# Performance work log

Measured on AMD Instinct MI355X. Metric: run time of the kernel, lower is better.

## Reference

```python
import jax, jax.numpy as jnp
import numpy as np

N_NODES = 100000
N_EDGES = 3200000
NCLASSES = 4
IN_DIM = 2          # per-node feature dim -> edge in_feats = 2*IN_DIM = 4
HID = 8             # output_dim


def setup_inputs() -> dict:
    key = jax.random.key(0)
    k_m, k_e, k_w1, k_b1, k_w2, k_b2 = jax.random.split(key, 6)
    m = jax.random.normal(k_m, (N_NODES, NCLASSES, IN_DIM), dtype=jnp.float32)
    edge_index = jax.random.randint(k_e, (2, N_EDGES), 0, N_NODES, dtype=jnp.int64)
    in_feats = 2 * IN_DIM
    # ClasswiseLinear: one independent Linear per class (grouped weights)
    s1 = 1.0 / np.sqrt(in_feats)
    s2 = 1.0 / np.sqrt(HID)
    W1 = jax.random.uniform(k_w1, (NCLASSES, in_feats, HID), jnp.float32, -s1, s1)
    b1 = jax.random.uniform(k_b1, (NCLASSES, HID), jnp.float32, -s1, s1)
    W2 = jax.random.uniform(k_w2, (NCLASSES, HID, 1), jnp.float32, -s2, s2)
    b2 = jax.random.uniform(k_b2, (NCLASSES, 1), jnp.float32, -s2, s2)
    return {"m": m, "edge_index": edge_index, "W1": W1, "b1": b1, "W2": W2, "b2": b2}


def reference(m, edge_index, W1, b1, W2, b2):
    row, col = edge_index[0], edge_index[1]
    # gather node features per edge; concat dest/src -> [E, C, 2*IN_DIM]
    B = jnp.concatenate([m[col], m[row]], axis=-1)
    B = jax.lax.stop_gradient(B)  # original code calls .detach()
    # classwise linear 1 + tanh: grouped GEMM over class axis c
    h = jnp.tanh(jnp.einsum("eci,cih->ech", B, W1) + b1)      # [E, C, HID]
    o = jnp.tanh(jnp.einsum("ech,cho->eco", h, W2) + b2)      # [E, C, 1]
    # softmax over the class dimension (dim=1)
    return jax.nn.softmax(o, axis=1)
```

## Files before the change

kernel.cpp:

```cpp
#include <hip/hip_runtime.h>

__device__ __forceinline__ float fast_tanh(float x) {
    float e = __builtin_amdgcn_exp2f(x * 2.8853901817779268f);
    float r = __builtin_amdgcn_rcpf(e + 1.0f);
    return fmaf(-2.0f, r, 1.0f);
}

__global__ __launch_bounds__(256) void edge_mlp(
    const float* __restrict__ m,
    const int*   __restrict__ eidx,
    const float* __restrict__ W1,
    const float* __restrict__ b1,
    const float* __restrict__ W2,
    const float* __restrict__ b2,
    float*       __restrict__ out,
    const int nE)
{
    const int tid0 = blockIdx.x * blockDim.x + threadIdx.x;
    const int c = tid0 & 3;

    float w1[32];
    #pragma unroll
    for (int k = 0; k < 8; ++k)
        *(float4*)(&w1[4*k]) = *(const float4*)(W1 + c*32 + 4*k);
    float bb1[8];
    *(float4*)(&bb1[0]) = *(const float4*)(b1 + c*8);
    *(float4*)(&bb1[4]) = *(const float4*)(b1 + c*8 + 4);
    float w2[8];
    *(float4*)(&w2[0]) = *(const float4*)(W2 + c*8);
    *(float4*)(&w2[4]) = *(const float4*)(W2 + c*8 + 4);
    const float b2s = b2[c];

    const int total  = nE * 4;
    const int stride = gridDim.x * blockDim.x;

    #pragma unroll 2
    for (int t = tid0; t < total; t += stride) {
        const int e   = t >> 2;
        const int row = eidx[e];
        const int col = eidx[nE + e];

        const float2 mc = *(const float2*)(m + (size_t)col * 8 + c * 2);
        const float2 mr = *(const float2*)(m + (size_t)row * 8 + c * 2);

        float o = b2s;
        #pragma unroll
        for (int j = 0; j < 8; ++j) {
            float h = bb1[j];
            h = fmaf(mc.x, w1[j],      h);
            h = fmaf(mc.y, w1[8 + j],  h);
            h = fmaf(mr.x, w1[16 + j], h);
            h = fmaf(mr.y, w1[24 + j], h);
            o = fmaf(fast_tanh(h), w2[j], o);
        }
        o = fast_tanh(o);

        const float eo = __builtin_amdgcn_exp2f(o * 1.4426950408889634f);
        float s = eo + __shfl_xor(eo, 1);
        s += __shfl_xor(s, 2);
        out[t] = eo * __builtin_amdgcn_rcpf(s);
    }
}

extern "C" void kernel_launch(void* const* d_in, const int* in_sizes, int n_in,
                              void* d_out, int out_size, void* d_ws, size_t ws_size,
                              hipStream_t stream) {
    const float* m  = (const float*)d_in[0];
    const int* eidx = (const int*)d_in[1];
    const float* W1 = (const float*)d_in[2];
    const float* b1 = (const float*)d_in[3];
    const float* W2 = (const float*)d_in[4];
    const float* b2 = (const float*)d_in[5];
    float* out = (float*)d_out;
    const int nE = in_sizes[1] / 2;

    const int threads = 256;
    const int blocks  = 2048;
    hipLaunchKernelGGL(edge_mlp, dim3(blocks), dim3(threads), 0, stream,
                       m, eidx, W1, b1, W2, b2, out, nE);
}
```

Before: 63.73 us.

## Process one edge per thread with all classes and vectorized node loads

Changes the mapping from one thread per (edge, class) to one thread per edge that computes all four classes. Each edge index is now loaded once instead of four times, node features are read as full float4 rows, and the output is written with a single nontemporal float4 store. The class softmax no longer needs cross-lane shuffles. Weights are now read from global memory as wave-uniform scalar loads rather than held per-lane in registers, and each thread does four times the arithmetic, which may raise register pressure and reduce available parallelism.

```diff
diff --git a/kernel.cpp b/kernel.cpp
--- a/kernel.cpp
+++ b/kernel.cpp
@@ -1,10 +1,9 @@
 #include <hip/hip_runtime.h>
 
-__device__ __forceinline__ float fast_tanh(float x) {
-    float e = __builtin_amdgcn_exp2f(x * 2.8853901817779268f);
-    float r = __builtin_amdgcn_rcpf(e + 1.0f);
-    return fmaf(-2.0f, r, 1.0f);
-}
+#define TWO_LOG2E 2.8853901817779268f
+#define LOG2E     1.4426950408889634f
+
+typedef float f32x4 __attribute__((ext_vector_type(4)));
 
 __global__ __launch_bounds__(256) void edge_mlp(
     const float* __restrict__ m,
@@ -16,49 +15,54 @@
     float*       __restrict__ out,
     const int nE)
 {
-    const int tid0 = blockIdx.x * blockDim.x + threadIdx.x;
-    const int c = tid0 & 3;
+    const int tid    = blockIdx.x * blockDim.x + threadIdx.x;
+    const int stride = gridDim.x * blockDim.x;
+    const int* eidx1 = eidx + nE;
 
-    float w1[32];
-    #pragma unroll
-    for (int k = 0; k < 8; ++k)
-        *(float4*)(&w1[4*k]) = *(const float4*)(W1 + c*32 + 4*k);
-    float bb1[8];
-    *(float4*)(&bb1[0]) = *(const float4*)(b1 + c*8);
-    *(float4*)(&bb1[4]) = *(const float4*)(b1 + c*8 + 4);
-    float w2[8];
-    *(float4*)(&w2[0]) = *(const float4*)(W2 + c*8);
-    *(float4*)(&w2[4]) = *(const float4*)(W2 + c*8 + 4);
-    const float b2s = b2[c];
+    for (int e0 = tid; e0 < nE; e0 += 2 * stride) {
+        #pragma unroll
+        for (int k = 0; k < 2; ++k) {
+            const int e = e0 + k * stride;
+            if (e >= nE) break;
+            const int r0 = __builtin_nontemporal_load(eidx  + e);
+            const int c0 = __builtin_nontemporal_load(eidx1 + e);
+            const f32x4 ca = *(const f32x4*)(m + (unsigned)c0 * 8u);
+            const f32x4 cb = *(const f32x4*)(m + (unsigned)c0 * 8u + 4);
+            const f32x4 ra = *(const f32x4*)(m + (unsigned)r0 * 8u);
+            const f32x4 rb = *(const f32x4*)(m + (unsigned)r0 * 8u + 4);
 
-    const int total  = nE * 4;
-    const int stride = gridDim.x * blockDim.x;
+            const float mcx[4] = {ca.x, ca.z, cb.x, cb.z};
+            const float mcy[4] = {ca.y, ca.w, cb.y, cb.w};
+            const float mrx[4] = {ra.x, ra.z, rb.x, rb.z};
+            const float mry[4] = {ra.y, ra.w, rb.y, rb.w};
 
-    #pragma unroll 2
-    for (int t = tid0; t < total; t += stride) {
-        const int e   = t >> 2;
-        const int row = eidx[e];
-        const int col = eidx[nE + e];
-
-        const float2 mc = *(const float2*)(m + (size_t)col * 8 + c * 2);
-        const float2 mr = *(const float2*)(m + (size_t)row * 8 + c * 2);
-
-        float o = b2s;
-        #pragma unroll
-        for (int j = 0; j < 8; ++j) {
-            float h = bb1[j];
-            h = fmaf(mc.x, w1[j],      h);
-            h = fmaf(mc.y, w1[8 + j],  h);
-            h = fmaf(mr.x, w1[16 + j], h);
-            h = fmaf(mr.y, w1[24 + j], h);
-            o = fmaf(fast_tanh(h), w2[j], o);
+            float eo[4];
+            float s = 0.0f;
+            #pragma unroll
+            for (int c = 0; c < 4; ++c) {
+                float o = b2[c];
+                #pragma unroll
+                for (int j = 0; j < 8; ++j) {
+                    float h = b1[c * 8 + j];
+                    h = fmaf(mcx[c], W1[c * 32 +      j], h);
+                    h = fmaf(mcy[c], W1[c * 32 +  8 + j], h);
+                    h = fmaf(mrx[c], W1[c * 32 + 16 + j], h);
+                    h = fmaf(mry[c], W1[c * 32 + 24 + j], h);
+                    const float ex = __builtin_amdgcn_exp2f(h * TWO_LOG2E);
+                    const float rr = __builtin_amdgcn_rcpf(ex + 1.0f);
+                    o = fmaf(fmaf(-2.0f, rr, 1.0f), W2[c * 8 + j], o);
+                }
+                const float e2 = __builtin_amdgcn_exp2f(o * TWO_LOG2E);
+                const float r2 = __builtin_amdgcn_rcpf(e2 + 1.0f);
+                eo[c] = __builtin_amdgcn_exp2f(fmaf(-TWO_LOG2E, r2, LOG2E));
+                s += eo[c];
+            }
+            const float rs = __builtin_amdgcn_rcpf(s);
+            f32x4 res;
+            res.x = eo[0] * rs; res.y = eo[1] * rs;
+            res.z = eo[2] * rs; res.w = eo[3] * rs;
+            __builtin_nontemporal_store(res, reinterpret_cast<f32x4*>(out) + e);
         }
-        o = fast_tanh(o);
-
-        const float eo = __builtin_amdgcn_exp2f(o * 1.4426950408889634f);
-        float s = eo + __shfl_xor(eo, 1);
-        s += __shfl_xor(s, 2);
-        out[t] = eo * __builtin_amdgcn_rcpf(s);
     }
 }
 
```

Result: slower. 70.18 us (+10.1%).
